# Kernel optimization log

Hardware: AMD Instinct MI355X
Metric: run time of the kernel (lower is better)

## Reference

```python
import jax, jax.numpy as jnp
import numpy as np

B, T, D, H = 8, 4096, 512, 512


def log_g(x):
    # log of g(x) where g(x) = relu(x) + 0.5 for x >= 0, sigmoid(x) for x < 0
    return jnp.where(x >= 0, jnp.log(jax.nn.relu(x) + 0.5), -jax.nn.softplus(-x))


def setup_inputs() -> dict:
    key = jax.random.key(0)
    kx, kh0, kwz, kbz, kwh, kbh = jax.random.split(key, 6)
    s = 1.0 / np.sqrt(D)
    return {
        "x": jax.random.normal(kx, (B, T, D), dtype=jnp.float32),
        "h_0": jax.random.uniform(kh0, (B, H), dtype=jnp.float32),
        "Wz": jax.random.uniform(kwz, (H, D), dtype=jnp.float32, minval=-s, maxval=s),
        "bz": jax.random.uniform(kbz, (H,), dtype=jnp.float32, minval=-s, maxval=s),
        "Wh": jax.random.uniform(kwh, (H, D), dtype=jnp.float32, minval=-s, maxval=s),
        "bh": jax.random.uniform(kbh, (H,), dtype=jnp.float32, minval=-s, maxval=s),
    }


def parallel_scan_log(log_coeffs, log_values):
    # log_coeffs: (B, T, H), log_values: (B, T+1, H)
    a_star = jnp.cumsum(jnp.pad(log_coeffs, ((0, 0), (1, 0), (0, 0))), axis=1)  # (B, T+1, H)
    log_h = a_star + jax.lax.cumlogsumexp(log_values - a_star, axis=1)
    return jnp.exp(log_h)  # (B, T+1, H)


def reference(x, h_0, Wz, bz, Wh, bh):
    k = jnp.einsum('btd,hd->bth', x, Wz) + bz                # (B, T, H)
    log_z = -jax.nn.softplus(-k)                              # log sigmoid(k)
    log_coeffs = -jax.nn.softplus(k)                          # log (1 - sigmoid(k))
    log_h0 = log_g(h_0)[:, None, :]                           # (B, 1, H)
    log_tilde_h = log_g(jnp.einsum('btd,hd->bth', x, Wh) + bh)
    vals = jnp.concatenate([log_h0, log_z + log_tilde_h], axis=1)  # (B, T+1, H)
    h = parallel_scan_log(log_coeffs, vals)
    return h[:, -x.shape[1]:, :]                              # (B, T, H)
```

## Files before the change

kernel.cpp:

```cpp
#include <hip/hip_runtime.h>
#include <math.h>

#define Bq 8
#define Tq 4096
#define Dq 512
#define Hq 512
#define Mq (Bq * Tq)
#define NC 64
#define CL 64
#define NP 1024

typedef unsigned short ushort_t;
typedef unsigned int uint_t;
typedef __bf16 bf16x8 __attribute__((ext_vector_type(8)));
typedef float f32x4 __attribute__((ext_vector_type(4)));

__device__ __forceinline__ ushort_t f2bf(float f) {
    unsigned int u = __float_as_uint(f);
    unsigned int r = u + 0x7fffu + ((u >> 16) & 1u);
    return (ushort_t)(r >> 16);
}

__device__ __forceinline__ void gload16(const void* g, void* l) {
    __builtin_amdgcn_global_load_lds(
        (const __attribute__((address_space(1))) void*)g,
        (__attribute__((address_space(3))) void*)l, 16, 0, 0);
}

__device__ __forceinline__ void gates(uint_t w, float& c, float& v) {
    float k  = __uint_as_float((w & 0xffffu) << 16);
    float th = __uint_as_float(w & 0xffff0000u);
    float ek = __expf(k);
    c = 1.0f / (1.0f + ek);
    float z = 1.0f - c;
    float g = (th >= 0.0f) ? (th + 0.5f) : (1.0f / (1.0f + __expf(-th)));
    v = z * g;
}

__global__ __launch_bounds__(256)
void convert_w(const float* __restrict__ Wz, const float* __restrict__ Wh,
               ushort_t* __restrict__ dst) {
    size_t i8 = ((size_t)blockIdx.x * 256 + threadIdx.x) * 8;
    int np = (int)(i8 >> 9);
    int d0 = (int)(i8 & (Dq - 1));
    int h  = ((np >> 5) << 4) | (np & 15);
    const float* src = ((np >> 4) & 1) ? Wh : Wz;
    src += (size_t)h * Dq + d0;
    float4 a = *reinterpret_cast<const float4*>(src);
    float4 b = *reinterpret_cast<const float4*>(src + 4);
    uint4 o;
    o.x = (uint_t)f2bf(a.x) | ((uint_t)f2bf(a.y) << 16);
    o.y = (uint_t)f2bf(a.z) | ((uint_t)f2bf(a.w) << 16);
    o.z = (uint_t)f2bf(b.x) | ((uint_t)f2bf(b.y) << 16);
    o.w = (uint_t)f2bf(b.z) | ((uint_t)f2bf(b.w) << 16);
    *reinterpret_cast<uint4*>(dst + i8) = o;
}

__global__ __launch_bounds__(256, 3)
void gemm_fused(const float* __restrict__ x, const ushort_t* __restrict__ wb,
                const float* __restrict__ bz, const float* __restrict__ bh,
                uint_t* __restrict__ kvout, float2* __restrict__ chAW) {
    __shared__ __align__(16) ushort_t smem[2 * 128 * 64];
    ushort_t* As = smem;
    ushort_t* Bs = smem + 128 * 64;

    const int logical = (blockIdx.x & 7) * 256 + (blockIdx.x >> 3);
    const int mBase = (logical >> 3) * 128;
    const int nBase = (logical & 7) * 128;

    const int tid  = threadIdx.x;
    const int lane = tid & 63;
    const int wave = tid >> 6;
    const int wm = (wave >> 1) * 64;
    const int wn = (wave & 1) * 64;

    f32x4 zero = {0.f, 0.f, 0.f, 0.f};
    f32x4 acc[4][4];
#pragma unroll
    for (int i = 0; i < 4; ++i)
#pragma unroll
        for (int j = 0; j < 4; ++j) acc[i][j] = zero;

    const int rowInW = lane >> 3;
    const int ccG = (lane & 7) ^ rowInW;
    const int swz = lane & 7;

    for (int k0 = 0; k0 < Dq; k0 += 64) {
#pragma unroll
        for (int j = 0; j < 4; ++j) {
            const int rseg = j * 4 + wave;
            const int row  = rseg * 8 + rowInW;
            const size_t gcol = (size_t)(k0 + ccG * 8);
            gload16(wb + (size_t)(nBase + row) * Dq + gcol, &Bs[rseg * 512]);
            const float* xs = x + (size_t)(mBase + row) * Dq + gcol;
            float4 a = *reinterpret_cast<const float4*>(xs);
            float4 b = *reinterpret_cast<const float4*>(xs + 4);
            uint4 o;
            o.x = (uint_t)f2bf(a.x) | ((uint_t)f2bf(a.y) << 16);
            o.y = (uint_t)f2bf(a.z) | ((uint_t)f2bf(a.w) << 16);
            o.z = (uint_t)f2bf(b.x) | ((uint_t)f2bf(b.y) << 16);
            o.w = (uint_t)f2bf(b.z) | ((uint_t)f2bf(b.w) << 16);
            *reinterpret_cast<uint4*>(As + rseg * 512 + lane * 8) = o;
        }
        __syncthreads();

#pragma unroll
        for (int ks = 0; ks < 2; ++ks) {
            const int cc = ks * 4 + (lane >> 4);
            const int sc = cc ^ swz;
            bf16x8 af[4], bf[4];
#pragma unroll
            for (int i = 0; i < 4; ++i) {
                int rowA = wm + i * 16 + (lane & 15);
                af[i] = *reinterpret_cast<const bf16x8*>(&As[rowA * 64 + sc * 8]);
                int rowB = wn + i * 16 + (lane & 15);
                bf[i] = *reinterpret_cast<const bf16x8*>(&Bs[rowB * 64 + sc * 8]);
            }
#pragma unroll
            for (int mi = 0; mi < 4; ++mi)
#pragma unroll
                for (int ni = 0; ni < 4; ++ni)
                    acc[mi][ni] = __builtin_amdgcn_mfma_f32_16x16x32_bf16(
                        af[mi], bf[ni], acc[mi][ni], 0, 0, 0);
        }
        __syncthreads();
    }

    const int colL = lane & 15;
    const int quad = lane >> 4;
    const int hOff = (nBase >> 1) + ((wave & 1) << 5);
    float2* sb = reinterpret_cast<float2*>(smem) + wave * 512;

#pragma unroll
    for (int q = 0; q < 2; ++q) {
        int h = hOff + q * 16 + colL;
        float bzv = bz[h];
        float bhv = bh[h];
#pragma unroll
        for (int mi = 0; mi < 4; ++mi) {
            float A = 1.f, W = 0.f;
#pragma unroll
            for (int r = 0; r < 4; ++r) {
                int bt = mBase + wm + mi * 16 + quad * 4 + r;
                float kf  = acc[mi][2 * q][r] + bzv;
                float thf = acc[mi][2 * q + 1][r] + bhv;
                uint_t word = (uint_t)f2bf(kf) | ((uint_t)f2bf(thf) << 16);
                kvout[(size_t)bt * Hq + h] = word;
                float c, v;
                gates(word, c, v);
                W = fmaf(c, W, v);
                A *= c;
            }
            sb[(mi * 4 + quad) * 32 + q * 16 + colL] = make_float2(A, W);
        }
    }
    __syncthreads();
    if (lane < 32) {
        float A = 1.f, W = 0.f;
#pragma unroll
        for (int s = 0; s < 16; ++s) {
            float2 aw = sb[s * 32 + lane];
            W = fmaf(aw.x, W, aw.y);
            A *= aw.x;
        }
        int g = (mBase >> 6) + (wm >> 6);
        int h = hOff + lane;
        chAW[(size_t)g * Hq + h] = make_float2(A, W);
    }
}

__global__ __launch_bounds__(512)
void scan_final(const uint_t* kv, const float* __restrict__ h0,
                const float2* __restrict__ chAW, float* out) {
    const int b = blockIdx.x & 7;
    const int chunk = 63 - (blockIdx.x >> 3);
    const int h = threadIdx.x;

    float x0 = h0[(size_t)b * Hq + h];
    float r = (x0 >= 0.f) ? (x0 + 0.5f) : (1.f / (1.f + __expf(-x0)));

    const float2* p = chAW + (size_t)b * NC * Hq + h;
    int j = 0;
    for (; j + 8 <= chunk; j += 8) {
        float2 aw[8];
#pragma unroll
        for (int q = 0; q < 8; ++q) aw[q] = p[(size_t)(j + q) * Hq];
#pragma unroll
        for (int q = 0; q < 8; ++q) r = fmaf(aw[q].x, r, aw[q].y);
    }
    for (; j < chunk; ++j) {
        float2 aw = p[(size_t)j * Hq];
        r = fmaf(aw.x, r, aw.y);
    }

    const size_t base = ((size_t)b * Tq + (size_t)chunk * CL) * Hq + h;
    const uint_t* kvp = kv + base;
    float* op = out + base;

    uint_t w[16];
#pragma unroll
    for (int q = 0; q < 16; ++q) w[q] = kvp[(size_t)q * Hq];
    for (int bt = 0; bt < 4; ++bt) {
        uint_t wn[16];
        if (bt < 3) {
#pragma unroll
            for (int q = 0; q < 16; ++q)
                wn[q] = kvp[(size_t)((bt + 1) * 16 + q) * Hq];
        }
#pragma unroll
        for (int q = 0; q < 16; ++q) {
            float c, v;
            gates(w[q], c, v);
            r = fmaf(c, r, v);
            op[(size_t)(bt * 16 + q) * Hq] = r;
        }
#pragma unroll
        for (int q = 0; q < 16; ++q) w[q] = wn[q];
    }
}

extern "C" void kernel_launch(void* const* d_in, const int* in_sizes, int n_in,
                              void* d_out, int out_size, void* d_ws, size_t ws_size,
                              hipStream_t stream) {
    const float* x  = (const float*)d_in[0];
    const float* h0 = (const float*)d_in[1];
    const float* Wz = (const float*)d_in[2];
    const float* bz = (const float*)d_in[3];
    const float* Wh = (const float*)d_in[4];
    const float* bh = (const float*)d_in[5];
    float* out = (float*)d_out;

    char* ws = (char*)d_ws;
    ushort_t* wb = (ushort_t*)ws;
    float2* chAW = (float2*)(wb + (size_t)NP * Dq);
    uint_t* kv = (uint_t*)d_out;

    const int wConv = (NP * Dq) / (256 * 8);
    convert_w<<<dim3(wConv), dim3(256), 0, stream>>>(Wz, Wh, wb);
    gemm_fused<<<dim3((Mq / 128) * (NP / 128)), dim3(256), 0, stream>>>(x, wb, bz, bh, kv, chAW);
    scan_final<<<dim3(Bq * NC), dim3(512), 0, stream>>>(kv, h0, chAW, out);
}
```

Before: 212.3 us.

## Pre-convert x to bf16 and use 256x256 pipelined GEMM with async LDS loads

x is now converted to bf16 in a separate pass together with the weights. The GEMM moves to 256x256 tiles with 8 waves, BK=32 and a 4-slot LDS ring filled by global_load_lds prefetch three steps ahead. It also uses explicit vmcnt waits, barriers and setprio around the MFMA blocks. This targets the per-tile fp32 load and convert stalls and raises arithmetic intensity, at the cost of an extra full read and write of x in bf16 (about 32MB extra traffic).

```diff
diff --git a/kernel.cpp b/kernel.cpp
--- a/kernel.cpp
+++ b/kernel.cpp
@@ -9,6 +9,8 @@
 #define NC 64
 #define CL 64
 #define NP 1024
+#define BKt 32
+#define NTt 16
 
 typedef unsigned short ushort_t;
 typedef unsigned int uint_t;
@@ -38,98 +40,128 @@
 }
 
 __global__ __launch_bounds__(256)
-void convert_w(const float* __restrict__ Wz, const float* __restrict__ Wh,
-               ushort_t* __restrict__ dst) {
+void convert_xw(const float* __restrict__ x, const float* __restrict__ Wz,
+                const float* __restrict__ Wh, ushort_t* __restrict__ xb,
+                ushort_t* __restrict__ wpb) {
     size_t i8 = ((size_t)blockIdx.x * 256 + threadIdx.x) * 8;
-    int np = (int)(i8 >> 9);
-    int d0 = (int)(i8 & (Dq - 1));
-    int h  = ((np >> 5) << 4) | (np & 15);
-    const float* src = ((np >> 4) & 1) ? Wh : Wz;
-    src += (size_t)h * Dq + d0;
-    float4 a = *reinterpret_cast<const float4*>(src);
-    float4 b = *reinterpret_cast<const float4*>(src + 4);
+    const size_t XN = (size_t)Mq * Dq;
+    const float* src; ushort_t* dst; size_t off;
+    if (i8 < XN) {
+        src = x; off = i8; dst = xb + i8;
+    } else {
+        size_t j8 = i8 - XN;
+        int np = (int)(j8 >> 9);
+        int d0 = (int)(j8 & (Dq - 1));
+        int h  = ((np >> 5) << 4) | (np & 15);
+        src = ((np >> 4) & 1) ? Wh : Wz;
+        off = (size_t)h * Dq + d0;
+        dst = wpb + j8;
+    }
+    float4 a = *reinterpret_cast<const float4*>(src + off);
+    float4 b = *reinterpret_cast<const float4*>(src + off + 4);
     uint4 o;
     o.x = (uint_t)f2bf(a.x) | ((uint_t)f2bf(a.y) << 16);
     o.y = (uint_t)f2bf(a.z) | ((uint_t)f2bf(a.w) << 16);
     o.z = (uint_t)f2bf(b.x) | ((uint_t)f2bf(b.y) << 16);
     o.w = (uint_t)f2bf(b.z) | ((uint_t)f2bf(b.w) << 16);
-    *reinterpret_cast<uint4*>(dst + i8) = o;
-}
-
-__global__ __launch_bounds__(256, 3)
-void gemm_fused(const float* __restrict__ x, const ushort_t* __restrict__ wb,
-                const float* __restrict__ bz, const float* __restrict__ bh,
-                uint_t* __restrict__ kvout, float2* __restrict__ chAW) {
-    __shared__ __align__(16) ushort_t smem[2 * 128 * 64];
-    ushort_t* As = smem;
-    ushort_t* Bs = smem + 128 * 64;
-
-    const int logical = (blockIdx.x & 7) * 256 + (blockIdx.x >> 3);
-    const int mBase = (logical >> 3) * 128;
-    const int nBase = (logical & 7) * 128;
+    *reinterpret_cast<uint4*>(dst) = o;
+}
+
+__global__ __launch_bounds__(512, 2)
+void gemm8(const ushort_t* __restrict__ xb, const ushort_t* __restrict__ wpb,
+           const float* __restrict__ bz, const float* __restrict__ bh,
+           uint_t* __restrict__ kvout, float2* __restrict__ chAW) {
+    __shared__ __align__(16) ushort_t smem[4 * 16384];
 
     const int tid  = threadIdx.x;
     const int lane = tid & 63;
     const int wave = tid >> 6;
-    const int wm = (wave >> 1) * 64;
-    const int wn = (wave & 1) * 64;
+    const int wave_m = wave >> 2;
+    const int wave_n = wave & 3;
+
+    const int logical = (blockIdx.x & 7) * 64 + (blockIdx.x >> 3);
+    const int mBase = (logical >> 2) * 256;
+    const int nBase = (logical & 3) * 256;
 
     f32x4 zero = {0.f, 0.f, 0.f, 0.f};
-    f32x4 acc[4][4];
-#pragma unroll
-    for (int i = 0; i < 4; ++i)
+    f32x4 acc[8][4];
+#pragma unroll
+    for (int i = 0; i < 8; ++i)
 #pragma unroll
         for (int j = 0; j < 4; ++j) acc[i][j] = zero;
 
-    const int rowInW = lane >> 3;
-    const int ccG = (lane & 7) ^ rowInW;
-    const int swz = lane & 7;
-
-    for (int k0 = 0; k0 < Dq; k0 += 64) {
-#pragma unroll
-        for (int j = 0; j < 4; ++j) {
-            const int rseg = j * 4 + wave;
-            const int row  = rseg * 8 + rowInW;
-            const size_t gcol = (size_t)(k0 + ccG * 8);
-            gload16(wb + (size_t)(nBase + row) * Dq + gcol, &Bs[rseg * 512]);
-            const float* xs = x + (size_t)(mBase + row) * Dq + gcol;
-            float4 a = *reinterpret_cast<const float4*>(xs);
-            float4 b = *reinterpret_cast<const float4*>(xs + 4);
-            uint4 o;
-            o.x = (uint_t)f2bf(a.x) | ((uint_t)f2bf(a.y) << 16);
-            o.y = (uint_t)f2bf(a.z) | ((uint_t)f2bf(a.w) << 16);
-            o.z = (uint_t)f2bf(b.x) | ((uint_t)f2bf(b.y) << 16);
-            o.w = (uint_t)f2bf(b.z) | ((uint_t)f2bf(b.w) << 16);
-            *reinterpret_cast<uint4*>(As + rseg * 512 + lane * 8) = o;
-        }
-        __syncthreads();
-
-#pragma unroll
-        for (int ks = 0; ks < 2; ++ks) {
-            const int cc = ks * 4 + (lane >> 4);
-            const int sc = cc ^ swz;
-            bf16x8 af[4], bf[4];
-#pragma unroll
-            for (int i = 0; i < 4; ++i) {
-                int rowA = wm + i * 16 + (lane & 15);
-                af[i] = *reinterpret_cast<const bf16x8*>(&As[rowA * 64 + sc * 8]);
-                int rowB = wn + i * 16 + (lane & 15);
-                bf[i] = *reinterpret_cast<const bf16x8*>(&Bs[rowB * 64 + sc * 8]);
-            }
-#pragma unroll
-            for (int mi = 0; mi < 4; ++mi)
-#pragma unroll
-                for (int ni = 0; ni < 4; ++ni)
-                    acc[mi][ni] = __builtin_amdgcn_mfma_f32_16x16x32_bf16(
-                        af[mi], bf[ni], acc[mi][ni], 0, 0, 0);
-        }
-        __syncthreads();
-    }
+    const ushort_t* srcA = xb  + (size_t)(mBase + (wave & 1) * 64 + lane) * Dq + (wave >> 1) * 8;
+    const ushort_t* srcB = wpb + (size_t)(nBase + (wave & 1) * 64 + lane) * Dq + (wave >> 1) * 8;
+    const int ldsW = wave * 512;
+
+    auto STAGE2 = [&](int t, int u0) {
+        ushort_t* slot = smem + (t & 3) * 16384;
+#pragma unroll
+        for (int u = 0; u < 2; ++u) {
+            const int uu = u0 + u;
+            const ushort_t* s = (uu < 2) ? (srcA + (size_t)(uu & 1) * 128 * Dq)
+                                         : (srcB + (size_t)(uu & 1) * 128 * Dq);
+            gload16(s + t * BKt, slot + uu * 4096 + ldsW);
+        }
+    };
+
+    STAGE2(0, 0); STAGE2(0, 2);
+    STAGE2(1, 0); STAGE2(1, 2);
+    STAGE2(2, 0); STAGE2(2, 2);
+    asm volatile("s_waitcnt vmcnt(8)" ::: "memory");
+    __builtin_amdgcn_s_barrier();
+    __builtin_amdgcn_sched_barrier(0);
+
+    const int aoff = wave_m * 4096 + (lane >> 4) * 1024 + (lane & 15) * 8;
+    const int boff = 8192 + (wave_n >> 1) * 4096 + (lane >> 4) * 1024
+                   + ((wave_n & 1) * 64 + (lane & 15)) * 8;
+
+    for (int t = 0; t < NTt; ++t) {
+        const ushort_t* slot = smem + (t & 3) * 16384;
+        bf16x8 bfr[4], afr[4];
+#pragma unroll
+        for (int ni = 0; ni < 4; ++ni)
+            bfr[ni] = *reinterpret_cast<const bf16x8*>(slot + boff + ni * 128);
+#pragma unroll
+        for (int i = 0; i < 4; ++i)
+            afr[i] = *reinterpret_cast<const bf16x8*>(slot + aoff + i * 128);
+        if (t + 3 < NTt) STAGE2(t + 3, 0);
+        __builtin_amdgcn_s_setprio(1);
+#pragma unroll
+        for (int mi = 0; mi < 4; ++mi)
+#pragma unroll
+            for (int ni = 0; ni < 4; ++ni)
+                acc[mi][ni] = __builtin_amdgcn_mfma_f32_16x16x32_bf16(
+                    afr[mi], bfr[ni], acc[mi][ni], 0, 0, 0);
+        __builtin_amdgcn_s_setprio(0);
+        __builtin_amdgcn_s_barrier();
+        __builtin_amdgcn_sched_barrier(0);
+#pragma unroll
+        for (int i = 0; i < 4; ++i)
+            afr[i] = *reinterpret_cast<const bf16x8*>(slot + aoff + (4 + i) * 128);
+        if (t + 3 < NTt) STAGE2(t + 3, 2);
+        __builtin_amdgcn_s_setprio(1);
+#pragma unroll
+        for (int mi = 0; mi < 4; ++mi)
+#pragma unroll
+            for (int ni = 0; ni < 4; ++ni)
+                acc[4 + mi][ni] = __builtin_amdgcn_mfma_f32_16x16x32_bf16(
+                    afr[mi], bfr[ni], acc[4 + mi][ni], 0, 0, 0);
+        __builtin_amdgcn_s_setprio(0);
+        if (t < NTt - 1) {
+            if (t < 13)       asm volatile("s_waitcnt vmcnt(8)" ::: "memory");
+            else if (t == 13) asm volatile("s_waitcnt vmcnt(4)" ::: "memory");
+            else              asm volatile("s_waitcnt vmcnt(0)" ::: "memory");
+            __builtin_amdgcn_s_barrier();
+            __builtin_amdgcn_sched_barrier(0);
+        }
+    }
+    __syncthreads();
 
     const int colL = lane & 15;
     const int quad = lane >> 4;
-    const int hOff = (nBase >> 1) + ((wave & 1) << 5);
-    float2* sb = reinterpret_cast<float2*>(smem) + wave * 512;
+    const int hOff = (nBase >> 1) + wave_n * 32;
+    float2* sb = reinterpret_cast<float2*>(smem) + wave * 1024;
 
 #pragma unroll
     for (int q = 0; q < 2; ++q) {
@@ -137,11 +169,11 @@
         float bzv = bz[h];
         float bhv = bh[h];
 #pragma unroll
-        for (int mi = 0; mi < 4; ++mi) {
+        for (int mi = 0; mi < 8; ++mi) {
             float A = 1.f, W = 0.f;
 #pragma unroll
             for (int r = 0; r < 4; ++r) {
-                int bt = mBase + wm + mi * 16 + quad * 4 + r;
+                int bt = mBase + wave_m * 128 + mi * 16 + quad * 4 + r;
                 float kf  = acc[mi][2 * q][r] + bzv;
                 float thf = acc[mi][2 * q + 1][r] + bhv;
                 uint_t word = (uint_t)f2bf(kf) | ((uint_t)f2bf(thf) << 16);
@@ -151,21 +183,24 @@
                 W = fmaf(c, W, v);
                 A *= c;
             }
-            sb[(mi * 4 + quad) * 32 + q * 16 + colL] = make_float2(A, W);
+            sb[(mi >> 2) * 512 + ((mi & 3) * 4 + quad) * 32 + q * 16 + colL] =
+                make_float2(A, W);
         }
     }
     __syncthreads();
-    if (lane < 32) {
+    {
+        int c  = lane >> 5;
+        int hh = lane & 31;
+        const float2* p = sb + c * 512;
         float A = 1.f, W = 0.f;
 #pragma unroll
         for (int s = 0; s < 16; ++s) {
-            float2 aw = sb[s * 32 + lane];
+            float2 aw = p[s * 32 + hh];
             W = fmaf(aw.x, W, aw.y);
             A *= aw.x;
         }
-        int g = (mBase >> 6) + (wm >> 6);
-        int h = hOff + lane;
-        chAW[(size_t)g * Hq + h] = make_float2(A, W);
+        int g = (mBase >> 6) + wave_m * 2 + c;
+        chAW[(size_t)g * Hq + hOff + hh] = make_float2(A, W);
     }
 }
 
@@ -231,12 +266,13 @@
     float* out = (float*)d_out;
 
     char* ws = (char*)d_ws;
-    ushort_t* wb = (ushort_t*)ws;
-    float2* chAW = (float2*)(wb + (size_t)NP * Dq);
+    ushort_t* xb = (ushort_t*)ws;
+    ushort_t* wpb = xb + (size_t)Mq * Dq;
+    float2* chAW = (float2*)(wpb + (size_t)NP * Dq);
     uint_t* kv = (uint_t*)d_out;
 
-    const int wConv = (NP * Dq) / (256 * 8);
-    convert_w<<<dim3(wConv), dim3(256), 0, stream>>>(Wz, Wh, wb);
-    gemm_fused<<<dim3((Mq / 128) * (NP / 128)), dim3(256), 0, stream>>>(x, wb, bz, bh, kv, chAW);
+    const int totalConv = (Mq * Dq + NP * Dq) / (256 * 8);
+    convert_xw<<<dim3(totalConv), dim3(256), 0, stream>>>(x, Wz, Wh, xb, wpb);
+    gemm8<<<dim3((Mq / 256) * (NP / 256)), dim3(512), 0, stream>>>(xb, wpb, bz, bh, kv, chAW);
     scan_final<<<dim3(Bq * NC), dim3(512), 0, stream>>>(kv, h0, chAW, out);
 }
```

New measurement: 209.7 us. No clear change (-1.2%).
